# Optimization experiments

Hardware: AMD Instinct MI355X
Metric: run time of the kernel (lower is better)

## Reference

```python
import jax, jax.numpy as jnp
import numpy as np

EPS = 1e-12  # F.normalize default eps


def setup_inputs() -> dict:
    key = jax.random.key(0)
    k1, k2 = jax.random.split(key)
    x = jax.random.normal(k1, (2, 96, 48, 48, 48), dtype=jnp.float32)  # backbone features [B,C,D,H,W]
    prototypes = jax.random.normal(k2, (512, 96), dtype=jnp.float32)   # nn.Parameter(512, 96)
    return {"x": x, "prototypes": prototypes}


def reference(x, prototypes):
    # F.normalize(x, dim=1): divide by max(||x||_2, eps) along channel dim
    xn = x / jnp.maximum(jnp.linalg.norm(x, axis=1, keepdims=True), EPS)
    xn = jnp.moveaxis(xn, 1, -1)  # [B, D, H, W, C]
    # F.normalize(prototypes, dim=1)
    pn = prototypes / jnp.maximum(jnp.linalg.norm(prototypes, axis=1, keepdims=True), EPS)
    # cosine similarity against all prototypes: [B, D, H, W, K]
    sims = jnp.einsum("bdhwc,kc->bdhwk", xn, pn)
    return jnp.argmax(sims, axis=-1)  # [B, D, H, W] int
```

## Files before the change

kernel.cpp:

```cpp
#include <hip/hip_runtime.h>
#include <math.h>

#define C 96
#define K 512
#define P_PER_B 110592
#define NPOS 221184
#define MT 64
#define ITERS_SIM 2
#define GRID_SIM 1728
#define CB 12


typedef _Float16 f16;
typedef _Float16 f16x8 __attribute__((ext_vector_type(8)));
typedef float f32x4 __attribute__((ext_vector_type(4)));


__global__ __launch_bounds__(256) void prep_kernel(const float* __restrict__ proto,
                                                   float* __restrict__ pnT,
                                                   f16* __restrict__ pn16h,
                                                   f16* __restrict__ pn16l) {
    int k = blockIdx.x * 256 + threadIdx.x;
    if (k >= K) return;
    const float* row = proto + k * C;
    float r[8];
#pragma unroll
    for (int j = 0; j < 8; ++j) r[j] = __fmul_rn(row[j], row[j]);
    for (int i = 8; i < C; i += 8) {
#pragma unroll
        for (int j = 0; j < 8; ++j)
            r[j] = __fadd_rn(r[j], __fmul_rn(row[i + j], row[i + j]));
    }
    float res = __fadd_rn(__fadd_rn(__fadd_rn(r[0], r[1]), __fadd_rn(r[2], r[3])),
                          __fadd_rn(__fadd_rn(r[4], r[5]), __fadd_rn(r[6], r[7])));
    float n = fmaxf(__fsqrt_rn(res), 1e-12f);
    for (int c = 0; c < C; ++c) {
        float v = __fdiv_rn(row[c], n);
        pnT[(size_t)c * K + k] = v;
        f16 h = (f16)v;
        pn16h[(size_t)k * C + c] = h;
        pn16l[(size_t)k * C + c] = (f16)(v - (float)h);
    }
}

__global__ __launch_bounds__(1024, 4) void sim_argmax_kernel(
        const float* __restrict__ x,
        const f16* __restrict__ pn16h,
        const f16* __restrict__ pn16l,
        int* __restrict__ out) {
    __shared__ __align__(16) f16 xth[CB * MT * 8];
    __shared__ __align__(16) f16 xtl[CB * MT * 8];
    __shared__ float n2p[CB][MT];
    __shared__ float wm1[16][MT], wm2[16][MT];

    const int tid = threadIdx.x;
    const int lane = tid & 63;
    const int w = tid >> 6;
    const int l15 = lane & 15;
    const int lg = lane >> 4;

    f16x8 afh[2][3], afl[2][3];
#pragma unroll
    for (int t = 0; t < 2; ++t)
#pragma unroll
        for (int q = 0; q < 3; ++q) {
            size_t off = (size_t)(w * 32 + t * 16 + l15) * C + q * 32 + lg * 8;
            afh[t][q] = *(const f16x8*)(pn16h + off);
            afl[t][q] = *(const f16x8*)(pn16l + off);
        }

    const int m00 = blockIdx.x * (MT * ITERS_SIM);
    const int b = (m00 >= P_PER_B) ? 1 : 0;
    const float* xq = x + (size_t)b * (size_t)C * P_PER_B + (m00 - b * P_PER_B)
                    + (size_t)(w << 3) * P_PER_B + lane;

#pragma unroll
    for (int it = 0; it < ITERS_SIM; ++it) {
        const int m0 = m00 + it * MT;

        __syncthreads();

        if (w < CB) {
            float ss = 0.f;
            f16x8 vh, vl;
#pragma unroll
            for (int j = 0; j < 8; ++j) {
                float v = xq[(size_t)j * P_PER_B + it * MT];
                ss = fmaf(v, v, ss);
                f16 h = (f16)v;
                vh[j] = h;
                vl[j] = (f16)(v - (float)h);
            }
            n2p[w][lane] = ss;
            *(f16x8*)(xth + ((w * MT + lane) << 3)) = vh;
            *(f16x8*)(xtl + ((w * MT + lane) << 3)) = vl;
        }
        __syncthreads();

        f32x4 acc[4][2];
#pragma unroll
        for (int s = 0; s < 4; ++s)
#pragma unroll
            for (int t = 0; t < 2; ++t)
                acc[s][t] = (f32x4){0.f, 0.f, 0.f, 0.f};
#pragma unroll
        for (int q = 0; q < 3; ++q) {
            const int cbase = ((q * 4 + lg) * MT) << 3;
            f16x8 bh[4], bl[4];
#pragma unroll
            for (int s = 0; s < 4; ++s)
                bh[s] = *(const f16x8*)(xth + cbase + ((s * 16 + l15) << 3));
#pragma unroll
            for (int s = 0; s < 4; ++s)
#pragma unroll
                for (int t = 0; t < 2; ++t)
                    acc[s][t] = __builtin_amdgcn_mfma_f32_16x16x32_f16(
                        afh[t][q], bh[s], acc[s][t], 0, 0, 0);
#pragma unroll
            for (int s = 0; s < 4; ++s)
                bl[s] = *(const f16x8*)(xtl + cbase + ((s * 16 + l15) << 3));
#pragma unroll
            for (int s = 0; s < 4; ++s)
#pragma unroll
                for (int t = 0; t < 2; ++t)
                    acc[s][t] = __builtin_amdgcn_mfma_f32_16x16x32_f16(
                        afl[t][q], bh[s], acc[s][t], 0, 0, 0);
#pragma unroll
            for (int s = 0; s < 4; ++s)
#pragma unroll
                for (int t = 0; t < 2; ++t)
                    acc[s][t] = __builtin_amdgcn_mfma_f32_16x16x32_f16(
                        afh[t][q], bl[s], acc[s][t], 0, 0, 0);
        }

        float m1[4], m2[4];
#pragma unroll
        for (int s = 0; s < 4; ++s) { m1[s] = -3.4e38f; m2[s] = -3.4e38f; }
        const int kb = w * 32 + (lg << 2);
#pragma unroll
        for (int t = 0; t < 2; ++t)
#pragma unroll
            for (int r = 0; r < 4; ++r) {
                const int kk = kb + t * 16 + r;
#pragma unroll
                for (int s = 0; s < 4; ++s) {
                    float v = acc[s][t][r];
                    float pk = __uint_as_float(
                        (__float_as_uint(v) & 0xFFFFFE00u) | (unsigned)kk);
                    m2[s] = fmaxf(m2[s], fminf(m1[s], pk));
                    m1[s] = fmaxf(m1[s], pk);
                }
            }

#pragma unroll
        for (int m = 16; m <= 32; m <<= 1)
#pragma unroll
            for (int s = 0; s < 4; ++s) {
                float o1 = __shfl_xor(m1[s], m);
                float o2 = __shfl_xor(m2[s], m);
                m2[s] = fmaxf(fmaxf(m2[s], o2), fminf(m1[s], o1));
                m1[s] = fmaxf(m1[s], o1);
            }
        if (lane < 16) {
#pragma unroll
            for (int s = 0; s < 4; ++s) {
                wm1[w][s * 16 + l15] = m1[s];
                wm2[w][s * 16 + l15] = m2[s];
            }
        }
        __syncthreads();

        if (tid < MT) {
            float n2 = 0.f;
#pragma unroll
            for (int g = 0; g < CB; ++g) n2 += n2p[g][tid];
            float b_ = wm1[0][tid], s_ = wm2[0][tid];
#pragma unroll
            for (int ww = 1; ww < 16; ++ww) {
                float o1 = wm1[ww][tid], o2 = wm2[ww][tid];
                s_ = fmaxf(fmaxf(s_, o2), fminf(b_, o1));
                b_ = fmaxf(b_, o1);
            }
            float tau = 2.6e-4f * sqrtf(n2) + 3e-5f;
            int k_ = (int)(__float_as_uint(b_) & 511u);
            out[m0 + tid] = (b_ - s_ < tau) ? (k_ | (int)0x80000000) : k_;
        }
    }
}

__global__ __launch_bounds__(256) void refine_kernel(
        const float* __restrict__ x,
        const float* __restrict__ pnT,
        int* __restrict__ out) {
    __shared__ int list[32];
    __shared__ int cnt;
    __shared__ float xn4[4][C];
    __shared__ float nrm4[4];

    const int tid = threadIdx.x;
    const int lane = tid & 63;
    const int w = tid >> 6;

    if (tid == 0) cnt = 0;
    __syncthreads();

    if (tid < 32) {
        int g = blockIdx.x * 32 + tid;
        if (out[g] < 0) {
            int i = atomicAdd(&cnt, 1);
            list[i] = g;
        }
    }
    __syncthreads();
    const int n = cnt;
    const int nmax = (n + 3) >> 2;

    for (int j = 0; j < nmax; ++j) {
        const int idx = j * 4 + w;
        const bool act = idx < n;
        const int gg = act ? list[idx] : list[0];
        const int b = (gg >= P_PER_B) ? 1 : 0;
        const int p = gg - b * P_PER_B;
        const float* xb = x + (size_t)b * (size_t)C * P_PER_B + p;

        if (act) {
            xn4[w][lane] = xb[(size_t)lane * P_PER_B];
            if (lane < C - 64) xn4[w][64 + lane] = xb[(size_t)(64 + lane) * P_PER_B];
        }
        __syncthreads();

        if (act && lane == 0) {
            float a = __fmul_rn(xn4[w][0], xn4[w][0]);
            for (int c = 1; c < C; ++c)
                a = __fadd_rn(a, __fmul_rn(xn4[w][c], xn4[w][c]));
            nrm4[w] = fmaxf(__fsqrt_rn(a), 1e-12f);
        }
        __syncthreads();
        if (act) {
            xn4[w][lane] = __fdiv_rn(xn4[w][lane], nrm4[w]);
            if (lane < C - 64)
                xn4[w][64 + lane] = __fdiv_rn(xn4[w][64 + lane], nrm4[w]);
        }
        __syncthreads();

        if (act) {
            float s[8];
#pragma unroll
            for (int r = 0; r < 8; ++r) s[r] = 0.f;
            for (int c = 0; c < C; ++c) {
                float xc = xn4[w][c];
                const float* pr = pnT + (size_t)c * K + lane;
#pragma unroll
                for (int r = 0; r < 8; ++r)
                    s[r] = __fadd_rn(s[r], __fmul_rn(xc, pr[r * 64]));
            }
            float bv = s[0];
            int bk = lane;
#pragma unroll
            for (int r = 1; r < 8; ++r) {
                if (s[r] > bv) { bv = s[r]; bk = lane + r * 64; }
            }
#pragma unroll
            for (int off = 1; off < 64; off <<= 1) {
                float ov = __shfl_xor(bv, off);
                int oi = __shfl_xor(bk, off);
                if (ov > bv || (ov == bv && oi < bk)) { bv = ov; bk = oi; }
            }
            if (lane == 0) out[gg] = bk;
        }
    }
}

extern "C" void kernel_launch(void* const* d_in, const int* in_sizes, int n_in,
                              void* d_out, int out_size, void* d_ws, size_t ws_size,
                              hipStream_t stream) {
    const float* x = (const float*)d_in[0];
    const float* proto = (const float*)d_in[1];
    int* out = (int*)d_out;

    float* pnT = (float*)d_ws;
    f16* pn16h = (f16*)((char*)d_ws + 196608);
    f16* pn16l = (f16*)((char*)d_ws + 294912);

    prep_kernel<<<2, 256, 0, stream>>>(proto, pnT, pn16h, pn16l);
    sim_argmax_kernel<<<GRID_SIM, 1024, 0, stream>>>(x, pn16h, pn16l, out);
    refine_kernel<<<NPOS / 32, 256, 0, stream>>>(x, pnT, out);
}
```

Measured before the change: 253.3 us.

## Prefetch next x tile into registers and reload low prototype fragments per chunk

Issues the global loads for the next iteration's x tile right after the LDS barrier, so they overlap the MFMA work, and holds them in registers. The low-half prototype fragments are no longer kept resident; they are reloaded from global memory for each K chunk to cut VGPR pressure under the 1024-thread launch bound. The MFMA sequence is regrouped into pairs of column tiles so fewer B fragments are live at once. The cost is extra global or cache traffic for the low prototype halves on every iteration.

```diff
diff --git a/kernel.cpp b/kernel.cpp
--- a/kernel.cpp
+++ b/kernel.cpp
@@ -59,21 +59,26 @@
     const int l15 = lane & 15;
     const int lg = lane >> 4;
 
-    f16x8 afh[2][3], afl[2][3];
-#pragma unroll
-    for (int t = 0; t < 2; ++t)
-#pragma unroll
-        for (int q = 0; q < 3; ++q) {
-            size_t off = (size_t)(w * 32 + t * 16 + l15) * C + q * 32 + lg * 8;
-            afh[t][q] = *(const f16x8*)(pn16h + off);
-            afl[t][q] = *(const f16x8*)(pn16l + off);
-        }
+    const size_t aoff0 = (size_t)(w * 32 + l15) * C + lg * 8;
+    const size_t aoff1 = aoff0 + (size_t)16 * C;
+    f16x8 afh0[3], afh1[3];
+#pragma unroll
+    for (int q = 0; q < 3; ++q) {
+        afh0[q] = *(const f16x8*)(pn16h + aoff0 + q * 32);
+        afh1[q] = *(const f16x8*)(pn16h + aoff1 + q * 32);
+    }
 
     const int m00 = blockIdx.x * (MT * ITERS_SIM);
     const int b = (m00 >= P_PER_B) ? 1 : 0;
     const float* xq = x + (size_t)b * (size_t)C * P_PER_B + (m00 - b * P_PER_B)
                     + (size_t)(w << 3) * P_PER_B + lane;
 
+    float fl[8];
+    if (w < CB) {
+#pragma unroll
+        for (int j = 0; j < 8; ++j) fl[j] = xq[(size_t)j * P_PER_B];
+    }
+
 #pragma unroll
     for (int it = 0; it < ITERS_SIM; ++it) {
         const int m0 = m00 + it * MT;
@@ -85,7 +90,7 @@
             f16x8 vh, vl;
 #pragma unroll
             for (int j = 0; j < 8; ++j) {
-                float v = xq[(size_t)j * P_PER_B + it * MT];
+                float v = fl[j];
                 ss = fmaf(v, v, ss);
                 f16 h = (f16)v;
                 vh[j] = h;
@@ -97,6 +102,12 @@
         }
         __syncthreads();
 
+        if (w < CB && it + 1 < ITERS_SIM) {
+#pragma unroll
+            for (int j = 0; j < 8; ++j)
+                fl[j] = xq[(size_t)j * P_PER_B + (it + 1) * MT];
+        }
+
         f32x4 acc[4][2];
 #pragma unroll
         for (int s = 0; s < 4; ++s)
@@ -106,31 +117,28 @@
 #pragma unroll
         for (int q = 0; q < 3; ++q) {
             const int cbase = ((q * 4 + lg) * MT) << 3;
-            f16x8 bh[4], bl[4];
-#pragma unroll
-            for (int s = 0; s < 4; ++s)
-                bh[s] = *(const f16x8*)(xth + cbase + ((s * 16 + l15) << 3));
-#pragma unroll
-            for (int s = 0; s < 4; ++s)
-#pragma unroll
-                for (int t = 0; t < 2; ++t)
-                    acc[s][t] = __builtin_amdgcn_mfma_f32_16x16x32_f16(
-                        afh[t][q], bh[s], acc[s][t], 0, 0, 0);
-#pragma unroll
-            for (int s = 0; s < 4; ++s)
-                bl[s] = *(const f16x8*)(xtl + cbase + ((s * 16 + l15) << 3));
-#pragma unroll
-            for (int s = 0; s < 4; ++s)
-#pragma unroll
-                for (int t = 0; t < 2; ++t)
-                    acc[s][t] = __builtin_amdgcn_mfma_f32_16x16x32_f16(
-                        afl[t][q], bh[s], acc[s][t], 0, 0, 0);
-#pragma unroll
-            for (int s = 0; s < 4; ++s)
-#pragma unroll
-                for (int t = 0; t < 2; ++t)
-                    acc[s][t] = __builtin_amdgcn_mfma_f32_16x16x32_f16(
-                        afh[t][q], bl[s], acc[s][t], 0, 0, 0);
+            f16x8 al0 = *(const f16x8*)(pn16l + aoff0 + q * 32);
+            f16x8 al1 = *(const f16x8*)(pn16l + aoff1 + q * 32);
+#pragma unroll
+            for (int sp = 0; sp < 2; ++sp) {
+                const int s0 = sp * 2, s1 = sp * 2 + 1;
+                f16x8 b0 = *(const f16x8*)(xth + cbase + ((s0 * 16 + l15) << 3));
+                f16x8 b1 = *(const f16x8*)(xth + cbase + ((s1 * 16 + l15) << 3));
+                acc[s0][0] = __builtin_amdgcn_mfma_f32_16x16x32_f16(afh0[q], b0, acc[s0][0], 0, 0, 0);
+                acc[s0][1] = __builtin_amdgcn_mfma_f32_16x16x32_f16(afh1[q], b0, acc[s0][1], 0, 0, 0);
+                acc[s1][0] = __builtin_amdgcn_mfma_f32_16x16x32_f16(afh0[q], b1, acc[s1][0], 0, 0, 0);
+                acc[s1][1] = __builtin_amdgcn_mfma_f32_16x16x32_f16(afh1[q], b1, acc[s1][1], 0, 0, 0);
+                acc[s0][0] = __builtin_amdgcn_mfma_f32_16x16x32_f16(al0, b0, acc[s0][0], 0, 0, 0);
+                acc[s0][1] = __builtin_amdgcn_mfma_f32_16x16x32_f16(al1, b0, acc[s0][1], 0, 0, 0);
+                acc[s1][0] = __builtin_amdgcn_mfma_f32_16x16x32_f16(al0, b1, acc[s1][0], 0, 0, 0);
+                acc[s1][1] = __builtin_amdgcn_mfma_f32_16x16x32_f16(al1, b1, acc[s1][1], 0, 0, 0);
+                f16x8 c0 = *(const f16x8*)(xtl + cbase + ((s0 * 16 + l15) << 3));
+                f16x8 c1 = *(const f16x8*)(xtl + cbase + ((s1 * 16 + l15) << 3));
+                acc[s0][0] = __builtin_amdgcn_mfma_f32_16x16x32_f16(afh0[q], c0, acc[s0][0], 0, 0, 0);
+                acc[s0][1] = __builtin_amdgcn_mfma_f32_16x16x32_f16(afh1[q], c0, acc[s0][1], 0, 0, 0);
+                acc[s1][0] = __builtin_amdgcn_mfma_f32_16x16x32_f16(afh0[q], c1, acc[s1][0], 0, 0, 0);
+                acc[s1][1] = __builtin_amdgcn_mfma_f32_16x16x32_f16(afh1[q], c1, acc[s1][1], 0, 0, 0);
+            }
         }
 
         float m1[4], m2[4];
```

New measurement: 236.4 us. 6.7% less time.

## Retile sim kernel to 512 threads with 64 prototypes per wave and fragment-ordered weights

Applied to the files above, without the earlier changes.

Halves the block to 8 waves, each now holding 64 prototypes (high parts in registers) against a 32-position tile, with four iterations per block. The low-part prototype fragments are streamed from global memory inside the MFMA loop instead of being kept in registers. Prep now writes prototype halves in an MFMA-fragment-contiguous layout so those loads coalesce. It also raises wave priority around the MFMA section and stops unrolling the outer loop. The aim is to cut register pressure and raise A-fragment reuse per wave, at the cost of extra global/L2 traffic for the low parts.

```diff
diff --git a/kernel.cpp b/kernel.cpp
--- a/kernel.cpp
+++ b/kernel.cpp
@@ -5,8 +5,8 @@
 #define K 512
 #define P_PER_B 110592
 #define NPOS 221184
-#define MT 64
-#define ITERS_SIM 2
+#define MT 32
+#define ITERS_SIM 4
 #define GRID_SIM 1728
 #define CB 12
 
@@ -15,6 +15,11 @@
 typedef _Float16 f16x8 __attribute__((ext_vector_type(8)));
 typedef float f32x4 __attribute__((ext_vector_type(4)));
 
+
+__device__ __forceinline__ size_t fidx(int k, int c) {
+    return (size_t)(((((k >> 4) * 3 + (c >> 5)) * 4 + ((c >> 3) & 3)) * 16
+                     + (k & 15)) * 8 + (c & 7));
+}
 
 __global__ __launch_bounds__(256) void prep_kernel(const float* __restrict__ proto,
                                                    float* __restrict__ pnT,
@@ -38,12 +43,13 @@
         float v = __fdiv_rn(row[c], n);
         pnT[(size_t)c * K + k] = v;
         f16 h = (f16)v;
-        pn16h[(size_t)k * C + c] = h;
-        pn16l[(size_t)k * C + c] = (f16)(v - (float)h);
-    }
-}
-
-__global__ __launch_bounds__(1024, 4) void sim_argmax_kernel(
+        size_t fi = fidx(k, c);
+        pn16h[fi] = h;
+        pn16l[fi] = (f16)(v - (float)h);
+    }
+}
+
+__global__ __launch_bounds__(512, 4) void sim_argmax_kernel(
         const float* __restrict__ x,
         const f16* __restrict__ pn16h,
         const f16* __restrict__ pn16l,
@@ -51,7 +57,7 @@
     __shared__ __align__(16) f16 xth[CB * MT * 8];
     __shared__ __align__(16) f16 xtl[CB * MT * 8];
     __shared__ float n2p[CB][MT];
-    __shared__ float wm1[16][MT], wm2[16][MT];
+    __shared__ float wm1[8][MT], wm2[8][MT];
 
     const int tid = threadIdx.x;
     const int lane = tid & 63;
@@ -59,28 +65,28 @@
     const int l15 = lane & 15;
     const int lg = lane >> 4;
 
-    f16x8 afh[2][3], afl[2][3];
-#pragma unroll
-    for (int t = 0; t < 2; ++t)
-#pragma unroll
-        for (int q = 0; q < 3; ++q) {
-            size_t off = (size_t)(w * 32 + t * 16 + l15) * C + q * 32 + lg * 8;
-            afh[t][q] = *(const f16x8*)(pn16h + off);
-            afl[t][q] = *(const f16x8*)(pn16l + off);
-        }
-
+    f16x8 afh[4][3];
+#pragma unroll
+    for (int t = 0; t < 4; ++t)
+#pragma unroll
+        for (int q = 0; q < 3; ++q)
+            afh[t][q] = *(const f16x8*)(pn16h
+                + (size_t)((((4 * w + t) * 3 + q) * 4 + lg) * 128 + l15 * 8));
+
+    const int cb = (w << 1) + (lane >> 5);
+    const int ps = lane & 31;
     const int m00 = blockIdx.x * (MT * ITERS_SIM);
     const int b = (m00 >= P_PER_B) ? 1 : 0;
     const float* xq = x + (size_t)b * (size_t)C * P_PER_B + (m00 - b * P_PER_B)
-                    + (size_t)(w << 3) * P_PER_B + lane;
-
-#pragma unroll
+                    + (size_t)(cb << 3) * P_PER_B + ps;
+
+#pragma unroll 1
     for (int it = 0; it < ITERS_SIM; ++it) {
         const int m0 = m00 + it * MT;
 
         __syncthreads();
 
-        if (w < CB) {
+        if (w < 6) {
             float ss = 0.f;
             f16x8 vh, vl;
 #pragma unroll
@@ -91,59 +97,62 @@
                 vh[j] = h;
                 vl[j] = (f16)(v - (float)h);
             }
-            n2p[w][lane] = ss;
-            *(f16x8*)(xth + ((w * MT + lane) << 3)) = vh;
-            *(f16x8*)(xtl + ((w * MT + lane) << 3)) = vl;
-        }
-        __syncthreads();
-
-        f32x4 acc[4][2];
-#pragma unroll
-        for (int s = 0; s < 4; ++s)
-#pragma unroll
-            for (int t = 0; t < 2; ++t)
+            n2p[cb][ps] = ss;
+            *(f16x8*)(xth + ((cb * MT + ps) << 3)) = vh;
+            *(f16x8*)(xtl + ((cb * MT + ps) << 3)) = vl;
+        }
+        __syncthreads();
+
+        f32x4 acc[2][4];
+#pragma unroll
+        for (int s = 0; s < 2; ++s)
+#pragma unroll
+            for (int t = 0; t < 4; ++t)
                 acc[s][t] = (f32x4){0.f, 0.f, 0.f, 0.f};
+
+        __builtin_amdgcn_s_setprio(1);
 #pragma unroll
         for (int q = 0; q < 3; ++q) {
             const int cbase = ((q * 4 + lg) * MT) << 3;
-            f16x8 bh[4], bl[4];
-#pragma unroll
-            for (int s = 0; s < 4; ++s)
-                bh[s] = *(const f16x8*)(xth + cbase + ((s * 16 + l15) << 3));
-#pragma unroll
-            for (int s = 0; s < 4; ++s)
-#pragma unroll
-                for (int t = 0; t < 2; ++t)
-                    acc[s][t] = __builtin_amdgcn_mfma_f32_16x16x32_f16(
-                        afh[t][q], bh[s], acc[s][t], 0, 0, 0);
-#pragma unroll
-            for (int s = 0; s < 4; ++s)
-                bl[s] = *(const f16x8*)(xtl + cbase + ((s * 16 + l15) << 3));
-#pragma unroll
-            for (int s = 0; s < 4; ++s)
-#pragma unroll
-                for (int t = 0; t < 2; ++t)
-                    acc[s][t] = __builtin_amdgcn_mfma_f32_16x16x32_f16(
-                        afl[t][q], bh[s], acc[s][t], 0, 0, 0);
-#pragma unroll
-            for (int s = 0; s < 4; ++s)
-#pragma unroll
-                for (int t = 0; t < 2; ++t)
-                    acc[s][t] = __builtin_amdgcn_mfma_f32_16x16x32_f16(
-                        afh[t][q], bl[s], acc[s][t], 0, 0, 0);
-        }
-
-        float m1[4], m2[4];
-#pragma unroll
-        for (int s = 0; s < 4; ++s) { m1[s] = -3.4e38f; m2[s] = -3.4e38f; }
-        const int kb = w * 32 + (lg << 2);
-#pragma unroll
-        for (int t = 0; t < 2; ++t)
+            f16x8 b0h = *(const f16x8*)(xth + cbase + (l15 << 3));
+            f16x8 b1h = *(const f16x8*)(xth + cbase + ((16 + l15) << 3));
+#pragma unroll
+            for (int tp = 0; tp < 2; ++tp) {
+                const int t0 = tp * 2, t1 = tp * 2 + 1;
+                f16x8 al0 = *(const f16x8*)(pn16l
+                    + (size_t)((((4 * w + t0) * 3 + q) * 4 + lg) * 128 + l15 * 8));
+                f16x8 al1 = *(const f16x8*)(pn16l
+                    + (size_t)((((4 * w + t1) * 3 + q) * 4 + lg) * 128 + l15 * 8));
+                acc[0][t0] = __builtin_amdgcn_mfma_f32_16x16x32_f16(afh[t0][q], b0h, acc[0][t0], 0, 0, 0);
+                acc[1][t0] = __builtin_amdgcn_mfma_f32_16x16x32_f16(afh[t0][q], b1h, acc[1][t0], 0, 0, 0);
+                acc[0][t1] = __builtin_amdgcn_mfma_f32_16x16x32_f16(afh[t1][q], b0h, acc[0][t1], 0, 0, 0);
+                acc[1][t1] = __builtin_amdgcn_mfma_f32_16x16x32_f16(afh[t1][q], b1h, acc[1][t1], 0, 0, 0);
+                acc[0][t0] = __builtin_amdgcn_mfma_f32_16x16x32_f16(al0, b0h, acc[0][t0], 0, 0, 0);
+                acc[1][t0] = __builtin_amdgcn_mfma_f32_16x16x32_f16(al0, b1h, acc[1][t0], 0, 0, 0);
+                acc[0][t1] = __builtin_amdgcn_mfma_f32_16x16x32_f16(al1, b0h, acc[0][t1], 0, 0, 0);
+                acc[1][t1] = __builtin_amdgcn_mfma_f32_16x16x32_f16(al1, b1h, acc[1][t1], 0, 0, 0);
+            }
+            f16x8 b0l = *(const f16x8*)(xtl + cbase + (l15 << 3));
+            f16x8 b1l = *(const f16x8*)(xtl + cbase + ((16 + l15) << 3));
+#pragma unroll
+            for (int t = 0; t < 4; ++t) {
+                acc[0][t] = __builtin_amdgcn_mfma_f32_16x16x32_f16(afh[t][q], b0l, acc[0][t], 0, 0, 0);
+                acc[1][t] = __builtin_amdgcn_mfma_f32_16x16x32_f16(afh[t][q], b1l, acc[1][t], 0, 0, 0);
+            }
+        }
+        __builtin_amdgcn_s_setprio(0);
+
+        float m1[2], m2[2];
+        m1[0] = m1[1] = -3.4e38f;
+        m2[0] = m2[1] = -3.4e38f;
+        const int kb = w * 64 + (lg << 2);
+#pragma unroll
+        for (int t = 0; t < 4; ++t)
 #pragma unroll
             for (int r = 0; r < 4; ++r) {
                 const int kk = kb + t * 16 + r;
 #pragma unroll
-                for (int s = 0; s < 4; ++s) {
+                for (int s = 0; s < 2; ++s) {
                     float v = acc[s][t][r];
                     float pk = __uint_as_float(
                         (__float_as_uint(v) & 0xFFFFFE00u) | (unsigned)kk);
@@ -155,18 +164,15 @@
 #pragma unroll
         for (int m = 16; m <= 32; m <<= 1)
 #pragma unroll
-            for (int s = 0; s < 4; ++s) {
+            for (int s = 0; s < 2; ++s) {
                 float o1 = __shfl_xor(m1[s], m);
                 float o2 = __shfl_xor(m2[s], m);
                 m2[s] = fmaxf(fmaxf(m2[s], o2), fminf(m1[s], o1));
                 m1[s] = fmaxf(m1[s], o1);
             }
         if (lane < 16) {
-#pragma unroll
-            for (int s = 0; s < 4; ++s) {
-                wm1[w][s * 16 + l15] = m1[s];
-                wm2[w][s * 16 + l15] = m2[s];
-            }
+            wm1[w][l15] = m1[0];      wm2[w][l15] = m2[0];
+            wm1[w][16 + l15] = m1[1]; wm2[w][16 + l15] = m2[1];
         }
         __syncthreads();
 
@@ -176,7 +182,7 @@
             for (int g = 0; g < CB; ++g) n2 += n2p[g][tid];
             float b_ = wm1[0][tid], s_ = wm2[0][tid];
 #pragma unroll
-            for (int ww = 1; ww < 16; ++ww) {
+            for (int ww = 1; ww < 8; ++ww) {
                 float o1 = wm1[ww][tid], o2 = wm2[ww][tid];
                 s_ = fmaxf(fmaxf(s_, o2), fminf(b_, o1));
                 b_ = fmaxf(b_, o1);
@@ -283,6 +289,6 @@
     f16* pn16l = (f16*)((char*)d_ws + 294912);
 
     prep_kernel<<<2, 256, 0, stream>>>(proto, pnT, pn16h, pn16l);
-    sim_argmax_kernel<<<GRID_SIM, 1024, 0, stream>>>(x, pn16h, pn16l, out);
+    sim_argmax_kernel<<<GRID_SIM, 512, 0, stream>>>(x, pn16h, pn16l, out);
     refine_kernel<<<NPOS / 32, 256, 0, stream>>>(x, pnT, out);
 }
```

Result: slower. 350.3 us (+38.3%).
